# Performance work log

Hardware: AMD Instinct MI355X
Metric: run time of the kernel (lower is better)

## Reference

```python
import jax, jax.numpy as jnp
import numpy as np
from jax import lax

TOP_K = 2
ROUTED_SCALING = 1.0
Q_MAX = 127.0


def setup_inputs() -> dict:
    key = jax.random.key(0)
    ks = jax.random.split(key, 7)
    B, S, H, I, E = 4, 2048, 2048, 1408, 8
    hidden_states = jax.random.normal(ks[0], (B, S, H), dtype=jnp.float32)
    gate_w = jax.random.normal(ks[1], (E, H), dtype=jnp.float32) * 0.02
    w13_q = jax.random.randint(ks[2], (E, 2 * I, H), -127, 128, dtype=jnp.int32)
    w13_scale = jax.random.uniform(ks[3], (E, 2 * I), dtype=jnp.float32, minval=0.5, maxval=1.5) * 0.01
    w2_q = jax.random.randint(ks[4], (E, H, I), -127, 128, dtype=jnp.int32)
    w2_scale = jax.random.uniform(ks[5], (E, H), dtype=jnp.float32, minval=0.5, maxval=1.5) * 0.01
    shared_output = jax.random.normal(ks[6], (B * S, H), dtype=jnp.float32)
    return {
        "hidden_states": hidden_states,
        "gate_w": gate_w,
        "w13_q": w13_q,
        "w13_scale": w13_scale,
        "w2_q": w2_q,
        "w2_scale": w2_scale,
        "shared_output": shared_output,
    }


def _dyn_quant_i8(x):
    """Per-token symmetric dynamic int8 quantization. Returns (q, scale)."""
    s = jnp.max(jnp.abs(x), axis=-1, keepdims=True) / Q_MAX
    s = jnp.maximum(s, 1e-8)
    q = jnp.clip(jnp.round(x / s), -Q_MAX, Q_MAX)
    return q, s


def reference(hidden_states, gate_w, w13_q, w13_scale, w2_q, w2_scale, shared_output):
    B, S, H = hidden_states.shape
    E = w13_q.shape[0]
    I = w2_q.shape[2]
    x = hidden_states.reshape(B * S, H)  # [T, H]

    # --- gating: fp32 linear + top-k softmax (renormalize=True) ---
    logits = jnp.einsum("th,eh->te", x, gate_w)
    probs = jax.nn.softmax(logits, axis=-1)
    gates, topk_idx = lax.top_k(probs, TOP_K)  # [T, K]
    gates = gates / jnp.sum(gates, axis=-1, keepdims=True)

    # --- dynamic per-token int8 quantization of activations ---
    xq, xs = _dyn_quant_i8(x)  # [T, H], [T, 1]

    # --- grouped int8 GEMM MoE, scanned over experts (faithful to
    # token-sorted grouped GEMM: each token is processed by each of its
    # top-k experts; here we compute per expert and mask/weight-combine). ---
    def body(acc, packed):
        w13_e, s13_e, w2_e, s2_e, e = packed
        # fc1 (w8a8, TN): dequant via per-token input scale * per-row weight scale
        h = (xq @ w13_e.astype(jnp.float32).T) * xs * s13_e[None, :]  # [T, 2I]
        # fused SwiGLU + dynamic int8 re-quant
        a = jax.nn.silu(h[:, :I]) * h[:, I:]
        aq, a_s = _dyn_quant_i8(a)
        # fc2 (w8a8, TN)
        y = (aq @ w2_e.astype(jnp.float32).T) * a_s * s2_e[None, :]  # [T, H]
        # gate weight for tokens routed to this expert (0 otherwise)
        w_tok = jnp.sum(jnp.where(topk_idx == e, gates, 0.0), axis=-1)  # [T]
        return acc + w_tok[:, None] * y, None

    acc0 = jnp.zeros((B * S, H), jnp.float32)
    acc, _ = lax.scan(body, acc0, (w13_q, w13_scale, w2_q, w2_scale, jnp.arange(E)))

    # --- combine: routed scaling + shared-expert residual ---
    return ROUTED_SCALING * acc + shared_output
```

## Files before the change

kernel.cpp:

```cpp
#include <hip/hip_runtime.h>
#include <math.h>

#define TOKS 8192
#define HD   2048
#define ID   1408
#define NE   8
#define N13  2816

typedef int v4i __attribute__((ext_vector_type(4)));

__global__ __launch_bounds__(256) void gate_quant_kernel(
    const float* __restrict__ x, const float* __restrict__ gw,
    signed char* __restrict__ xq, float* __restrict__ xs,
    float* __restrict__ gates, int* __restrict__ counts, int* __restrict__ lists)
{
    const int t = blockIdx.x;
    const int tid = threadIdx.x;
    const float* xr = x + (size_t)t * HD + tid * 8;
    const float4 xa = *(const float4*)(xr);
    const float4 xb = *(const float4*)(xr + 4);
    float acc[NE];
#pragma unroll
    for (int e = 0; e < NE; ++e) {
        const float* wr = gw + e * HD + tid * 8;
        float4 wa = *(const float4*)(wr);
        float4 wb = *(const float4*)(wr + 4);
        acc[e] = xa.x*wa.x + xa.y*wa.y + xa.z*wa.z + xa.w*wa.w +
                 xb.x*wb.x + xb.y*wb.y + xb.z*wb.z + xb.w*wb.w;
    }
    float am = fmaxf(fmaxf(fmaxf(fabsf(xa.x), fabsf(xa.y)), fmaxf(fabsf(xa.z), fabsf(xa.w))),
                     fmaxf(fmaxf(fabsf(xb.x), fabsf(xb.y)), fmaxf(fabsf(xb.z), fabsf(xb.w))));
#pragma unroll
    for (int off = 1; off < 64; off <<= 1) {
#pragma unroll
        for (int e = 0; e < NE; ++e) acc[e] += __shfl_xor(acc[e], off);
        am = fmaxf(am, __shfl_xor(am, off));
    }
    __shared__ float red[4][9];
    __shared__ float sbc;
    const int wv = tid >> 6;
    if ((tid & 63) == 0) {
#pragma unroll
        for (int e = 0; e < NE; ++e) red[wv][e] = acc[e];
        red[wv][8] = am;
    }
    __syncthreads();
    if (tid == 0) {
        float l[NE];
#pragma unroll
        for (int e = 0; e < NE; ++e) l[e] = red[0][e] + red[1][e] + red[2][e] + red[3][e];
        float amx = fmaxf(fmaxf(red[0][8], red[1][8]), fmaxf(red[2][8], red[3][8]));
        int e0 = 0;
#pragma unroll
        for (int e = 1; e < NE; ++e) if (l[e] > l[e0]) e0 = e;
        int e1 = (e0 == 0) ? 1 : 0;
#pragma unroll
        for (int e = 0; e < NE; ++e) if (e != e0 && l[e] > l[e1]) e1 = e;
        const float d = expf(l[e1] - l[e0]);
        gates[2*t]     = 1.0f / (1.0f + d);
        gates[2*t + 1] = d / (1.0f + d);
        const int p0 = atomicAdd(&counts[e0], 1); lists[e0*TOKS + p0] = 2*t;
        const int p1 = atomicAdd(&counts[e1], 1); lists[e1*TOKS + p1] = 2*t + 1;
        const float s = fmaxf(amx / 127.0f, 1e-8f);
        xs[t] = s;
        sbc = s;
    }
    __syncthreads();
    const float s = sbc;
    const float v[8] = {xa.x, xa.y, xa.z, xa.w, xb.x, xb.y, xb.z, xb.w};
    unsigned int lo = 0, hi = 0;
#pragma unroll
    for (int i = 0; i < 4; ++i) {
        int q = (int)fminf(fmaxf(rintf(v[i] / s), -127.f), 127.f);
        lo |= ((unsigned)(q & 0xff)) << (8 * i);
    }
#pragma unroll
    for (int i = 0; i < 4; ++i) {
        int q = (int)fminf(fmaxf(rintf(v[4 + i] / s), -127.f), 127.f);
        hi |= ((unsigned)(q & 0xff)) << (8 * i);
    }
    int2 pk; pk.x = (int)lo; pk.y = (int)hi;
    *(int2*)(xq + (size_t)t * HD + tid * 8) = pk;
}

__global__ __launch_bounds__(256) void convert_w13_kernel(
    const int* __restrict__ wq, signed char* __restrict__ w8)
{
    const unsigned idx = blockIdx.x * 256u + threadIdx.x;
    const unsigned kq = idx & 511u;
    const unsigned rowq = idx >> 9;
    const unsigned np = rowq % 2816u;
    const unsigned e = rowq / 2816u;
    const unsigned inrow = ((np >> 4) & 1u) * 1408u + (np >> 5) * 16u + (np & 15u);
    const int4 vv = *(const int4*)(wq + (size_t)(e * 2816u + inrow) * 2048u + kq * 4u);
    char4 c;
    c.x = (signed char)vv.x; c.y = (signed char)vv.y;
    c.z = (signed char)vv.z; c.w = (signed char)vv.w;
    *(char4*)(w8 + (size_t)rowq * 2048u + kq * 4u) = c;
}

__global__ __launch_bounds__(256) void convert_w2_kernel(
    const int* __restrict__ wq, signed char* __restrict__ w8)
{
    const size_t idx = (size_t)blockIdx.x * 256 + threadIdx.x;
    const int4 vv = *(const int4*)(wq + idx * 4);
    char4 c;
    c.x = (signed char)vv.x; c.y = (signed char)vv.y;
    c.z = (signed char)vv.z; c.w = (signed char)vv.w;
    *(char4*)(w8 + idx * 4) = c;
}

__global__ __launch_bounds__(256) void copy_out_kernel(
    const float* __restrict__ src, float* __restrict__ dst)
{
    const size_t idx = (size_t)blockIdx.x * 256 + threadIdx.x;
    ((float4*)dst)[idx] = ((const float4*)src)[idx];
}

__global__ __launch_bounds__(256, 2) void fc1_kernel(
    const signed char* __restrict__ xq, const signed char* __restrict__ w13_8,
    const float* __restrict__ xs, const float* __restrict__ w13s,
    const int* __restrict__ counts, const int* __restrict__ lists,
    float* __restrict__ a_buf, unsigned int* __restrict__ amax)
{
    const int e = blockIdx.z;
    const int n_e = counts[e];
    const int m0 = blockIdx.y * 128;
    if (m0 >= n_e) return;
    const int n0 = blockIdx.x * 128;
    const int* list = lists + e * TOKS;
    const signed char* B = w13_8 + (size_t)e * N13 * HD;

    __shared__ signed char lsA[128 * 80];
    __shared__ signed char lsB[128 * 80];

    const int tid = threadIdx.x;
    const int srow = tid >> 1, shalf = tid & 1;
    const int aidx = m0 + srow;
    const int aslot = (aidx < n_e) ? list[aidx] : 0;
    const signed char* Aptr = xq + (size_t)(aslot >> 1) * HD + shalf * 32;
    const signed char* Bptr = B + (size_t)(n0 + srow) * HD + shalf * 32;
    signed char* wA = lsA + srow * 80 + shalf * 32;
    signed char* wB = lsB + srow * 80 + shalf * 32;

    const int lane = tid & 63;
    const int wv = tid >> 6;
    const int quad = lane >> 4, jj = lane & 15;
    const int wm = (wv >> 1) * 64, wn = (wv & 1) * 64;

    const v4i zero = {0, 0, 0, 0};
    v4i acc[4][4];
#pragma unroll
    for (int a = 0; a < 4; ++a)
#pragma unroll
        for (int b = 0; b < 4; ++b) acc[a][b] = zero;

    for (int kc = 0; kc < 32; ++kc) {
        const int k0 = kc * 64;
        const int4 a0 = *(const int4*)(Aptr + k0);
        const int4 a1 = *(const int4*)(Aptr + k0 + 16);
        const int4 b0 = *(const int4*)(Bptr + k0);
        const int4 b1 = *(const int4*)(Bptr + k0 + 16);
        __syncthreads();
        *(int4*)(wA) = a0;
        *(int4*)(wA + 16) = a1;
        *(int4*)(wB) = b0;
        *(int4*)(wB + 16) = b1;
        __syncthreads();
        v4i af[4], bf[4];
#pragma unroll
        for (int mi = 0; mi < 4; ++mi)
            af[mi] = *(const v4i*)(lsA + (wm + mi * 16 + jj) * 80 + quad * 16);
#pragma unroll
        for (int ni = 0; ni < 4; ++ni)
            bf[ni] = *(const v4i*)(lsB + (wn + ni * 16 + jj) * 80 + quad * 16);
#pragma unroll
        for (int mi = 0; mi < 4; ++mi)
#pragma unroll
            for (int ni = 0; ni < 4; ++ni)
                acc[mi][ni] = __builtin_amdgcn_mfma_i32_16x16x64_i8(af[mi], bf[ni], acc[mi][ni], 0, 0, 0);
    }

    const float* s13e = w13s + e * N13;
    const int qbase = (n0 + wn) >> 5;
#pragma unroll
    for (int mi = 0; mi < 4; ++mi) {
#pragma unroll
        for (int r = 0; r < 4; ++r) {
            const int idx = m0 + wm + mi * 16 + quad * 4 + r;
            const bool valid = (idx < n_e);
            int slot = 0; float xsv = 0.f;
            if (valid) { slot = list[idx]; xsv = xs[slot >> 1]; }
            float rowmax = 0.f;
            float avals[2];
#pragma unroll
            for (int p = 0; p < 2; ++p) {
                const int q = qbase + p;
                const float sg = s13e[q * 16 + jj];
                const float su = s13e[ID + q * 16 + jj];
                const float hg = (float)acc[mi][2 * p][r] * xsv * sg;
                const float hu = (float)acc[mi][2 * p + 1][r] * xsv * su;
                const float av = hg / (1.0f + expf(-hg)) * hu;
                avals[p] = av;
                rowmax = fmaxf(rowmax, fabsf(av));
            }
            rowmax = fmaxf(rowmax, __shfl_xor(rowmax, 1));
            rowmax = fmaxf(rowmax, __shfl_xor(rowmax, 2));
            rowmax = fmaxf(rowmax, __shfl_xor(rowmax, 4));
            rowmax = fmaxf(rowmax, __shfl_xor(rowmax, 8));
            if (valid) {
                float* arow = a_buf + (size_t)slot * ID;
#pragma unroll
                for (int p = 0; p < 2; ++p) arow[(qbase + p) * 16 + jj] = avals[p];
                if (jj == 0) atomicMax(amax + slot, __float_as_uint(rowmax));
            }
        }
    }
}

__global__ __launch_bounds__(256) void requant_kernel(
    const float* __restrict__ a_buf, const unsigned int* __restrict__ amax,
    float* __restrict__ a_s, signed char* __restrict__ aq)
{
    const int row = blockIdx.x;
    const float am = __uint_as_float(amax[row]);
    const float s = fmaxf(am / 127.0f, 1e-8f);
    if (threadIdx.x == 0) a_s[row] = s;
    const float* ar = a_buf + (size_t)row * ID;
    signed char* qr = aq + (size_t)row * ID;
    for (int c = threadIdx.x; c < ID / 4; c += 256) {
        const float4 v = *(const float4*)(ar + c * 4);
        char4 o;
        o.x = (signed char)(int)fminf(fmaxf(rintf(v.x / s), -127.f), 127.f);
        o.y = (signed char)(int)fminf(fmaxf(rintf(v.y / s), -127.f), 127.f);
        o.z = (signed char)(int)fminf(fmaxf(rintf(v.z / s), -127.f), 127.f);
        o.w = (signed char)(int)fminf(fmaxf(rintf(v.w / s), -127.f), 127.f);
        *(char4*)(qr + c * 4) = o;
    }
}

__global__ __launch_bounds__(256, 2) void fc2_kernel(
    const signed char* __restrict__ aq, const signed char* __restrict__ w2_8,
    const float* __restrict__ a_s, const float* __restrict__ w2s,
    const float* __restrict__ gates,
    const int* __restrict__ counts, const int* __restrict__ lists,
    float* __restrict__ out)
{
    const int e = blockIdx.z;
    const int n_e = counts[e];
    const int m0 = blockIdx.y * 128;
    if (m0 >= n_e) return;
    const int n0 = blockIdx.x * 128;
    const int* list = lists + e * TOKS;
    const signed char* B = w2_8 + (size_t)e * HD * ID;

    __shared__ signed char lsA[128 * 80];
    __shared__ signed char lsB[128 * 80];

    const int tid = threadIdx.x;
    const int srow = tid >> 1, shalf = tid & 1;
    const int aidx = m0 + srow;
    const int aslot = (aidx < n_e) ? list[aidx] : 0;
    const signed char* Aptr = aq + (size_t)aslot * ID + shalf * 32;
    const signed char* Bptr = B + (size_t)(n0 + srow) * ID + shalf * 32;
    signed char* wA = lsA + srow * 80 + shalf * 32;
    signed char* wB = lsB + srow * 80 + shalf * 32;

    const int lane = tid & 63;
    const int wv = tid >> 6;
    const int quad = lane >> 4, jj = lane & 15;
    const int wm = (wv >> 1) * 64, wn = (wv & 1) * 64;

    const v4i zero = {0, 0, 0, 0};
    v4i acc[4][4];
#pragma unroll
    for (int a = 0; a < 4; ++a)
#pragma unroll
        for (int b = 0; b < 4; ++b) acc[a][b] = zero;

    for (int kc = 0; kc < 22; ++kc) {
        const int k0 = kc * 64;
        const int4 a0 = *(const int4*)(Aptr + k0);
        const int4 a1 = *(const int4*)(Aptr + k0 + 16);
        const int4 b0 = *(const int4*)(Bptr + k0);
        const int4 b1 = *(const int4*)(Bptr + k0 + 16);
        __syncthreads();
        *(int4*)(wA) = a0;
        *(int4*)(wA + 16) = a1;
        *(int4*)(wB) = b0;
        *(int4*)(wB + 16) = b1;
        __syncthreads();
        v4i af[4], bf[4];
#pragma unroll
        for (int mi = 0; mi < 4; ++mi)
            af[mi] = *(const v4i*)(lsA + (wm + mi * 16 + jj) * 80 + quad * 16);
#pragma unroll
        for (int ni = 0; ni < 4; ++ni)
            bf[ni] = *(const v4i*)(lsB + (wn + ni * 16 + jj) * 80 + quad * 16);
#pragma unroll
        for (int mi = 0; mi < 4; ++mi)
#pragma unroll
            for (int ni = 0; ni < 4; ++ni)
                acc[mi][ni] = __builtin_amdgcn_mfma_i32_16x16x64_i8(af[mi], bf[ni], acc[mi][ni], 0, 0, 0);
    }

    const float* s2e = w2s + e * HD;
    float s2v[4];
#pragma unroll
    for (int ni = 0; ni < 4; ++ni) s2v[ni] = s2e[n0 + wn + ni * 16 + jj];
#pragma unroll
    for (int mi = 0; mi < 4; ++mi) {
#pragma unroll
        for (int r = 0; r < 4; ++r) {
            const int idx = m0 + wm + mi * 16 + quad * 4 + r;
            if (idx >= n_e) continue;
            const int slot = list[idx];
            const float coef = a_s[slot] * gates[slot];
            float* orow = out + (size_t)(slot >> 1) * HD + n0 + wn;
#pragma unroll
            for (int ni = 0; ni < 4; ++ni)
                atomicAdd(orow + ni * 16 + jj, (float)acc[mi][ni][r] * coef * s2v[ni]);
        }
    }
}

extern "C" void kernel_launch(void* const* d_in, const int* in_sizes, int n_in,
                              void* d_out, int out_size, void* d_ws, size_t ws_size,
                              hipStream_t stream)
{
    const float* x      = (const float*)d_in[0];
    const float* gw     = (const float*)d_in[1];
    const int*   w13q   = (const int*)d_in[2];
    const float* w13s   = (const float*)d_in[3];
    const int*   w2q    = (const int*)d_in[4];
    const float* w2s    = (const float*)d_in[5];
    const float* shared = (const float*)d_in[6];
    float* out = (float*)d_out;
    char* ws = (char*)d_ws;

    constexpr size_t SZ_W13 = (size_t)NE * N13 * HD;
    constexpr size_t SZ_W2  = (size_t)NE * HD * ID;
    constexpr size_t SZ_XQ  = (size_t)TOKS * HD;
    constexpr size_t SZ_AQ  = (size_t)2 * TOKS * ID;
    constexpr size_t SZ_A   = SZ_AQ * 4;
    constexpr size_t OFF_W13 = 0;
    constexpr size_t OFF_W2  = OFF_W13 + SZ_W13;
    constexpr size_t OFF_XQ  = OFF_W2 + SZ_W2;
    constexpr size_t OFF_AQ  = OFF_XQ + SZ_XQ;
    constexpr size_t OFF_A   = OFF_AQ + SZ_AQ;
    constexpr size_t OFF_XS  = OFF_A + SZ_A;
    constexpr size_t OFF_AS  = OFF_XS + 65536;
    constexpr size_t OFF_G   = OFF_AS + 65536;
    constexpr size_t OFF_AM  = OFF_G + 65536;
    constexpr size_t OFF_CNT = OFF_AM + 65536;
    constexpr size_t OFF_LST = OFF_CNT + 256;

    signed char* w13_8 = (signed char*)(ws + OFF_W13);
    signed char* w2_8  = (signed char*)(ws + OFF_W2);
    signed char* xq    = (signed char*)(ws + OFF_XQ);
    signed char* aqb   = (signed char*)(ws + OFF_AQ);
    float* a_buf = (float*)(ws + OFF_A);
    float* xs    = (float*)(ws + OFF_XS);
    float* a_s   = (float*)(ws + OFF_AS);
    float* gates = (float*)(ws + OFF_G);
    unsigned int* amax = (unsigned int*)(ws + OFF_AM);
    int* counts = (int*)(ws + OFF_CNT);
    int* lists  = (int*)(ws + OFF_LST);

    hipMemsetAsync(counts, 0, 256, stream);
    hipMemsetAsync(amax, 0, 65536, stream);

    gate_quant_kernel<<<TOKS, 256, 0, stream>>>(x, gw, xq, xs, gates, counts, lists);
    convert_w13_kernel<<<(NE * N13 * (HD / 4)) / 256, 256, 0, stream>>>(w13q, w13_8);
    convert_w2_kernel<<<(NE * HD * (ID / 4)) / 256, 256, 0, stream>>>(w2q, w2_8);
    copy_out_kernel<<<(TOKS * HD / 4) / 256, 256, 0, stream>>>(shared, out);
    fc1_kernel<<<dim3(N13 / 128, 64, NE), 256, 0, stream>>>(
        xq, w13_8, xs, w13s, counts, lists, a_buf, amax);
    requant_kernel<<<2 * TOKS, 256, 0, stream>>>(a_buf, amax, a_s, aqb);
    fc2_kernel<<<dim3(HD / 128, 64, NE), 256, 0, stream>>>(
        aqb, w2_8, a_s, w2s, gates, counts, lists, out);
}
```

Before: 947.9 us.

## Use direct global-to-LDS async loads with XOR swizzle and bf16 intermediate buffer

Replaces the register-staged global→LDS copies in the fc1 and fc2 int8 GEMMs with global_load_lds direct copies, using an unpadded 64-byte-row LDS layout with an XOR swizzle to avoid bank conflicts. Stores the SwiGLU intermediate in bf16 instead of fp32, halving the write and read traffic between fc1 and requant, and vectorizes requant to 8 elements per thread. This risks small numerical differences from bf16 rounding before re-quantization. It also depends on the swizzle matching the layout global_load_lds writes per wave.

```diff
diff --git a/kernel.cpp b/kernel.cpp
--- a/kernel.cpp
+++ b/kernel.cpp
@@ -1,4 +1,5 @@
 #include <hip/hip_runtime.h>
+#include <hip/hip_bf16.h>
 #include <math.h>
 
 #define TOKS 8192
@@ -8,6 +9,12 @@
 #define N13  2816
 
 typedef int v4i __attribute__((ext_vector_type(4)));
+
+__device__ __forceinline__ void async_copy16(const signed char* g, signed char* l) {
+    __builtin_amdgcn_global_load_lds(
+        (const __attribute__((address_space(1))) void*)g,
+        (__attribute__((address_space(3))) void*)l, 16, 0, 0);
+}
 
 __global__ __launch_bounds__(256) void gate_quant_kernel(
     const float* __restrict__ x, const float* __restrict__ gw,
@@ -121,7 +128,7 @@
     const signed char* __restrict__ xq, const signed char* __restrict__ w13_8,
     const float* __restrict__ xs, const float* __restrict__ w13s,
     const int* __restrict__ counts, const int* __restrict__ lists,
-    float* __restrict__ a_buf, unsigned int* __restrict__ amax)
+    __hip_bfloat16* __restrict__ a_buf, unsigned int* __restrict__ amax)
 {
     const int e = blockIdx.z;
     const int n_e = counts[e];
@@ -131,22 +138,32 @@
     const int* list = lists + e * TOKS;
     const signed char* B = w13_8 + (size_t)e * N13 * HD;
 
-    __shared__ signed char lsA[128 * 80];
-    __shared__ signed char lsB[128 * 80];
+    __shared__ signed char lsA[128 * 64];
+    __shared__ signed char lsB[128 * 64];
 
     const int tid = threadIdx.x;
-    const int srow = tid >> 1, shalf = tid & 1;
-    const int aidx = m0 + srow;
-    const int aslot = (aidx < n_e) ? list[aidx] : 0;
-    const signed char* Aptr = xq + (size_t)(aslot >> 1) * HD + shalf * 32;
-    const signed char* Bptr = B + (size_t)(n0 + srow) * HD + shalf * 32;
-    signed char* wA = lsA + srow * 80 + shalf * 32;
-    signed char* wB = lsB + srow * 80 + shalf * 32;
-
-    const int lane = tid & 63;
     const int wv = tid >> 6;
-    const int quad = lane >> 4, jj = lane & 15;
+    const int l  = tid & 63;
+    const int r4 = l >> 2;
+    const int c4 = l & 3;
+    const int k16 = c4 ^ (r4 & 3);
+
+    const int rowA0 = m0 + wv * 32 + r4;
+    const int rowA1 = rowA0 + 16;
+    const int slotA0 = (rowA0 < n_e) ? list[rowA0] : 0;
+    const int slotA1 = (rowA1 < n_e) ? list[rowA1] : 0;
+    const signed char* gA0 = xq + (size_t)(slotA0 >> 1) * HD + k16 * 16;
+    const signed char* gA1 = xq + (size_t)(slotA1 >> 1) * HD + k16 * 16;
+    const signed char* gB0 = B + (size_t)(n0 + wv * 32 + r4) * HD + k16 * 16;
+    const signed char* gB1 = gB0 + (size_t)16 * HD;
+    signed char* ldsA0 = lsA + (wv * 2 + 0) * 1024;
+    signed char* ldsA1 = lsA + (wv * 2 + 1) * 1024;
+    signed char* ldsB0 = lsB + (wv * 2 + 0) * 1024;
+    signed char* ldsB1 = lsB + (wv * 2 + 1) * 1024;
+
+    const int quad = l >> 4, jj = l & 15;
     const int wm = (wv >> 1) * 64, wn = (wv & 1) * 64;
+    const int swz = ((quad ^ (jj & 3)) * 16);
 
     const v4i zero = {0, 0, 0, 0};
     v4i acc[4][4];
@@ -157,23 +174,19 @@
 
     for (int kc = 0; kc < 32; ++kc) {
         const int k0 = kc * 64;
-        const int4 a0 = *(const int4*)(Aptr + k0);
-        const int4 a1 = *(const int4*)(Aptr + k0 + 16);
-        const int4 b0 = *(const int4*)(Bptr + k0);
-        const int4 b1 = *(const int4*)(Bptr + k0 + 16);
         __syncthreads();
-        *(int4*)(wA) = a0;
-        *(int4*)(wA + 16) = a1;
-        *(int4*)(wB) = b0;
-        *(int4*)(wB + 16) = b1;
+        async_copy16(gA0 + k0, ldsA0);
+        async_copy16(gA1 + k0, ldsA1);
+        async_copy16(gB0 + k0, ldsB0);
+        async_copy16(gB1 + k0, ldsB1);
         __syncthreads();
         v4i af[4], bf[4];
 #pragma unroll
         for (int mi = 0; mi < 4; ++mi)
-            af[mi] = *(const v4i*)(lsA + (wm + mi * 16 + jj) * 80 + quad * 16);
+            af[mi] = *(const v4i*)(lsA + (wm + mi * 16 + jj) * 64 + swz);
 #pragma unroll
         for (int ni = 0; ni < 4; ++ni)
-            bf[ni] = *(const v4i*)(lsB + (wn + ni * 16 + jj) * 80 + quad * 16);
+            bf[ni] = *(const v4i*)(lsB + (wn + ni * 16 + jj) * 64 + swz);
 #pragma unroll
         for (int mi = 0; mi < 4; ++mi)
 #pragma unroll
@@ -209,33 +222,45 @@
             rowmax = fmaxf(rowmax, __shfl_xor(rowmax, 4));
             rowmax = fmaxf(rowmax, __shfl_xor(rowmax, 8));
             if (valid) {
-                float* arow = a_buf + (size_t)slot * ID;
-#pragma unroll
-                for (int p = 0; p < 2; ++p) arow[(qbase + p) * 16 + jj] = avals[p];
+                __hip_bfloat16* arow = a_buf + (size_t)slot * ID;
+#pragma unroll
+                for (int p = 0; p < 2; ++p)
+                    arow[(qbase + p) * 16 + jj] = __float2bfloat16(avals[p]);
                 if (jj == 0) atomicMax(amax + slot, __float_as_uint(rowmax));
             }
         }
     }
 }
 
-__global__ __launch_bounds__(256) void requant_kernel(
-    const float* __restrict__ a_buf, const unsigned int* __restrict__ amax,
+__global__ __launch_bounds__(192) void requant_kernel(
+    const __hip_bfloat16* __restrict__ a_buf, const unsigned int* __restrict__ amax,
     float* __restrict__ a_s, signed char* __restrict__ aq)
 {
     const int row = blockIdx.x;
     const float am = __uint_as_float(amax[row]);
     const float s = fmaxf(am / 127.0f, 1e-8f);
     if (threadIdx.x == 0) a_s[row] = s;
-    const float* ar = a_buf + (size_t)row * ID;
+    const unsigned short* ar = (const unsigned short*)(a_buf + (size_t)row * ID);
     signed char* qr = aq + (size_t)row * ID;
-    for (int c = threadIdx.x; c < ID / 4; c += 256) {
-        const float4 v = *(const float4*)(ar + c * 4);
-        char4 o;
-        o.x = (signed char)(int)fminf(fmaxf(rintf(v.x / s), -127.f), 127.f);
-        o.y = (signed char)(int)fminf(fmaxf(rintf(v.y / s), -127.f), 127.f);
-        o.z = (signed char)(int)fminf(fmaxf(rintf(v.z / s), -127.f), 127.f);
-        o.w = (signed char)(int)fminf(fmaxf(rintf(v.w / s), -127.f), 127.f);
-        *(char4*)(qr + c * 4) = o;
+    const float inv = 1.0f / s;
+    for (int c = threadIdx.x; c < ID / 8; c += 192) {
+        union { int4 v; unsigned short u[8]; } dat;
+        dat.v = *(const int4*)(ar + c * 8);
+        unsigned int lo = 0, hi = 0;
+#pragma unroll
+        for (int i = 0; i < 4; ++i) {
+            const float f = __uint_as_float((unsigned)dat.u[i] << 16);
+            int q = (int)fminf(fmaxf(rintf(f * inv), -127.f), 127.f);
+            lo |= ((unsigned)(q & 0xff)) << (8 * i);
+        }
+#pragma unroll
+        for (int i = 0; i < 4; ++i) {
+            const float f = __uint_as_float((unsigned)dat.u[4 + i] << 16);
+            int q = (int)fminf(fmaxf(rintf(f * inv), -127.f), 127.f);
+            hi |= ((unsigned)(q & 0xff)) << (8 * i);
+        }
+        int2 pk; pk.x = (int)lo; pk.y = (int)hi;
+        *(int2*)(qr + c * 8) = pk;
     }
 }
 
@@ -254,22 +279,32 @@
     const int* list = lists + e * TOKS;
     const signed char* B = w2_8 + (size_t)e * HD * ID;
 
-    __shared__ signed char lsA[128 * 80];
-    __shared__ signed char lsB[128 * 80];
+    __shared__ signed char lsA[128 * 64];
+    __shared__ signed char lsB[128 * 64];
 
     const int tid = threadIdx.x;
-    const int srow = tid >> 1, shalf = tid & 1;
-    const int aidx = m0 + srow;
-    const int aslot = (aidx < n_e) ? list[aidx] : 0;
-    const signed char* Aptr = aq + (size_t)aslot * ID + shalf * 32;
-    const signed char* Bptr = B + (size_t)(n0 + srow) * ID + shalf * 32;
-    signed char* wA = lsA + srow * 80 + shalf * 32;
-    signed char* wB = lsB + srow * 80 + shalf * 32;
-
-    const int lane = tid & 63;
     const int wv = tid >> 6;
-    const int quad = lane >> 4, jj = lane & 15;
+    const int l  = tid & 63;
+    const int r4 = l >> 2;
+    const int c4 = l & 3;
+    const int k16 = c4 ^ (r4 & 3);
+
+    const int rowA0 = m0 + wv * 32 + r4;
+    const int rowA1 = rowA0 + 16;
+    const int slotA0 = (rowA0 < n_e) ? list[rowA0] : 0;
+    const int slotA1 = (rowA1 < n_e) ? list[rowA1] : 0;
+    const signed char* gA0 = aq + (size_t)slotA0 * ID + k16 * 16;
+    const signed char* gA1 = aq + (size_t)slotA1 * ID + k16 * 16;
+    const signed char* gB0 = B + (size_t)(n0 + wv * 32 + r4) * ID + k16 * 16;
+    const signed char* gB1 = gB0 + (size_t)16 * ID;
+    signed char* ldsA0 = lsA + (wv * 2 + 0) * 1024;
+    signed char* ldsA1 = lsA + (wv * 2 + 1) * 1024;
+    signed char* ldsB0 = lsB + (wv * 2 + 0) * 1024;
+    signed char* ldsB1 = lsB + (wv * 2 + 1) * 1024;
+
+    const int quad = l >> 4, jj = l & 15;
     const int wm = (wv >> 1) * 64, wn = (wv & 1) * 64;
+    const int swz = ((quad ^ (jj & 3)) * 16);
 
     const v4i zero = {0, 0, 0, 0};
     v4i acc[4][4];
@@ -280,23 +315,19 @@
 
     for (int kc = 0; kc < 22; ++kc) {
         const int k0 = kc * 64;
-        const int4 a0 = *(const int4*)(Aptr + k0);
-        const int4 a1 = *(const int4*)(Aptr + k0 + 16);
-        const int4 b0 = *(const int4*)(Bptr + k0);
-        const int4 b1 = *(const int4*)(Bptr + k0 + 16);
         __syncthreads();
-        *(int4*)(wA) = a0;
-        *(int4*)(wA + 16) = a1;
-        *(int4*)(wB) = b0;
-        *(int4*)(wB + 16) = b1;
+        async_copy16(gA0 + k0, ldsA0);
+        async_copy16(gA1 + k0, ldsA1);
+        async_copy16(gB0 + k0, ldsB0);
+        async_copy16(gB1 + k0, ldsB1);
         __syncthreads();
         v4i af[4], bf[4];
 #pragma unroll
         for (int mi = 0; mi < 4; ++mi)
-            af[mi] = *(const v4i*)(lsA + (wm + mi * 16 + jj) * 80 + quad * 16);
+            af[mi] = *(const v4i*)(lsA + (wm + mi * 16 + jj) * 64 + swz);
 #pragma unroll
         for (int ni = 0; ni < 4; ++ni)
-            bf[ni] = *(const v4i*)(lsB + (wn + ni * 16 + jj) * 80 + quad * 16);
+            bf[ni] = *(const v4i*)(lsB + (wn + ni * 16 + jj) * 64 + swz);
 #pragma unroll
         for (int mi = 0; mi < 4; ++mi)
 #pragma unroll
@@ -342,7 +373,7 @@
     constexpr size_t SZ_W2  = (size_t)NE * HD * ID;
     constexpr size_t SZ_XQ  = (size_t)TOKS * HD;
     constexpr size_t SZ_AQ  = (size_t)2 * TOKS * ID;
-    constexpr size_t SZ_A   = SZ_AQ * 4;
+    constexpr size_t SZ_A   = SZ_AQ * 2;
     constexpr size_t OFF_W13 = 0;
     constexpr size_t OFF_W2  = OFF_W13 + SZ_W13;
     constexpr size_t OFF_XQ  = OFF_W2 + SZ_W2;
@@ -359,7 +390,7 @@
     signed char* w2_8  = (signed char*)(ws + OFF_W2);
     signed char* xq    = (signed char*)(ws + OFF_XQ);
     signed char* aqb   = (signed char*)(ws + OFF_AQ);
-    float* a_buf = (float*)(ws + OFF_A);
+    __hip_bfloat16* a_buf = (__hip_bfloat16*)(ws + OFF_A);
     float* xs    = (float*)(ws + OFF_XS);
     float* a_s   = (float*)(ws + OFF_AS);
     float* gates = (float*)(ws + OFF_G);
@@ -376,7 +407,7 @@
     copy_out_kernel<<<(TOKS * HD / 4) / 256, 256, 0, stream>>>(shared, out);
     fc1_kernel<<<dim3(N13 / 128, 64, NE), 256, 0, stream>>>(
         xq, w13_8, xs, w13s, counts, lists, a_buf, amax);
-    requant_kernel<<<2 * TOKS, 256, 0, stream>>>(a_buf, amax, a_s, aqb);
+    requant_kernel<<<2 * TOKS, 192, 0, stream>>>(a_buf, amax, a_s, aqb);
     fc2_kernel<<<dim3(HD / 128, 64, NE), 256, 0, stream>>>(
         aqb, w2_8, a_s, w2s, gates, counts, lists, out);
 }
```

Result: faster. 920.8 us (-2.9%).
